# Kernel optimization log

Measured on AMD Instinct MI355X. Metric: run time of the kernel, lower is better.

The kernel has to match this reference:

```python
import jax, jax.numpy as jnp
import numpy as np

B, D, L = 16, 64, 1280
H = 8            # nhead
WIN = 5          # window_size (divides L exactly)
DFF = 128        # dim_feedforward
EPS = 1e-5


def _layernorm(x, g, b):
    mu = jnp.mean(x, axis=-1, keepdims=True)
    var = jnp.mean(jnp.square(x - mu), axis=-1, keepdims=True)
    return (x - mu) * jax.lax.rsqrt(var + EPS) * g + b


def _mha(x, w_in, b_in, w_out, b_out):
    # x: (Bx, Lx, D). torch nn.MultiheadAttention, batch_first, eval mode.
    Bx, Lx, Dm = x.shape
    hd = Dm // H
    qkv = x @ w_in.T + b_in                      # (Bx, Lx, 3D)
    q, k, v = jnp.split(qkv, 3, axis=-1)
    q = q.reshape(Bx, Lx, H, hd)
    k = k.reshape(Bx, Lx, H, hd)
    v = v.reshape(Bx, Lx, H, hd)
    scale = 1.0 / jnp.sqrt(jnp.asarray(hd, x.dtype))
    scores = jnp.einsum('bqhd,bkhd->bhqk', q, k) * scale
    att = jax.nn.softmax(scores, axis=-1)
    out = jnp.einsum('bhqk,bkhd->bqhd', att, v).reshape(Bx, Lx, Dm)
    return out @ w_out.T + b_out


def setup_inputs() -> dict:
    key = jax.random.key(0)
    ks = jax.random.split(key, 16)
    s = 0.05
    return {
        'x': jax.random.normal(ks[0], (B, D, L), dtype=jnp.float32),
        # local attention params
        'lw_in': jax.random.normal(ks[1], (3 * D, D), dtype=jnp.float32) * s,
        'lb_in': jnp.zeros((3 * D,), jnp.float32),
        'lw_out': jax.random.normal(ks[2], (D, D), dtype=jnp.float32) * s,
        'lb_out': jnp.zeros((D,), jnp.float32),
        # global attention params
        'gw_in': jax.random.normal(ks[3], (3 * D, D), dtype=jnp.float32) * s,
        'gb_in': jnp.zeros((3 * D,), jnp.float32),
        'gw_out': jax.random.normal(ks[4], (D, D), dtype=jnp.float32) * s,
        'gb_out': jnp.zeros((D,), jnp.float32),
        # gating weight (init 0.5 like the module)
        'local_weight': jnp.full((D,), 0.5, jnp.float32),
        # layer norms
        'g1': jnp.ones((D,), jnp.float32), 'b1': jnp.zeros((D,), jnp.float32),
        'g2': jnp.ones((D,), jnp.float32), 'b2': jnp.zeros((D,), jnp.float32),
        'g3': jnp.ones((D,), jnp.float32), 'b3': jnp.zeros((D,), jnp.float32),
        # FFN
        'w1': jax.random.normal(ks[5], (DFF, D), dtype=jnp.float32) * s,
        'bf1': jnp.zeros((DFF,), jnp.float32),
        'w2': jax.random.normal(ks[6], (D, DFF), dtype=jnp.float32) * s,
        'bf2': jnp.zeros((D,), jnp.float32),
    }


def reference(x, lw_in, lb_in, lw_out, lb_out, gw_in, gb_in, gw_out, gb_out,
              local_weight, g1, b1, g2, b2, g3, b3, w1, bf1, w2, bf2):
    xt = jnp.transpose(x, (0, 2, 1))              # (B, L, D)
    residual = xt
    nW = L // WIN
    xw = xt.reshape(B * nW, WIN, D)
    local_out = _mha(xw, lw_in, lb_in, lw_out, lb_out).reshape(B, L, D)
    local_out = _layernorm(local_out + residual, g1, b1)
    # global attention
    global_out = _mha(xt, gw_in, gb_in, gw_out, gb_out)
    global_out = _layernorm(global_out + residual, g2, b2)
    # gated channel fusion
    alpha = jax.nn.sigmoid(local_weight)[None, None, :]
    fused = alpha * local_out + (1.0 - alpha) * global_out
    # FFN (dropout is identity in eval mode)
    ffn_out = jax.nn.relu(fused @ w1.T + bf1) @ w2.T + bf2
    out = _layernorm(ffn_out + fused, g3, b3)
    return jnp.transpose(out, (0, 2, 1))          # (B, D, L)
```

## Files before the change

### kernel.cpp

```cpp
#include <hip/hip_runtime.h>
#include <math.h>

typedef short bf16x8 __attribute__((ext_vector_type(8)));
typedef float f32x4 __attribute__((ext_vector_type(4)));
typedef unsigned short u16;
typedef unsigned int u32;

#define RFL(x) __builtin_amdgcn_readfirstlane(x)

static __device__ __forceinline__ float bf2f(u16 s) {
  union { u32 u; float f; } c; c.u = ((u32)s) << 16; return c.f;
}
static __device__ __forceinline__ u16 f2bf(float f) {
  union { float f; u32 u; } c; c.f = f;
  u32 u = c.u + 0x7fffu + ((c.u >> 16) & 1u);
  return (u16)(u >> 16);
}
static __device__ __forceinline__ u32 pk2(float lo, float hi) {
  u32 r;
  asm("v_cvt_pk_bf16_f32 %0, %1, %2" : "=v"(r) : "v"(lo), "v"(hi));
  return r;
}
static __device__ __forceinline__ f32x4 MF(bf16x8 a, bf16x8 b, f32x4 c) {
  return __builtin_amdgcn_mfma_f32_16x16x32_bf16(a, b, c, 0, 0, 0);
}


__global__ __launch_bounds__(256) void qkvx(
    const float* __restrict__ x, const float* __restrict__ lw_in,
    const float* __restrict__ gw_in, const float* __restrict__ lb_in,
    const float* __restrict__ gb_in, u16* __restrict__ QKV) {
  __shared__ __align__(16) float xs[32][68];
  __shared__ __align__(16) u16 XTs[32 * 64];
  const int t = threadIdx.x;
  const int b = blockIdx.x / 40, l0 = (blockIdx.x % 40) * 32;
  for (int i = t; i < 2048; i += 256) {
    const int d = i >> 5, tok = i & 31;
    xs[tok][d] = x[(b * 64 + d) * 1280 + l0 + tok];
  }
  __syncthreads();
  {
    const int tok = t >> 3, c8 = (t & 7) * 8;
    union { bf16x8 v; u32 u[4]; } o;
    const float* src = &xs[tok][c8];
    o.u[0] = pk2(src[0], src[1]); o.u[1] = pk2(src[2], src[3]);
    o.u[2] = pk2(src[4], src[5]); o.u[3] = pk2(src[6], src[7]);
    const int byteoff = (tok * 128 + c8 * 2) ^ ((tok & 7) << 4);
    *(bf16x8*)((char*)XTs + byteoff) = o.v;
  }
  __syncthreads();
  const int lane = t & 63, w = RFL(t >> 6);
  const int lr = lane & 15, lg = lane >> 4;
  const int n0 = w * 96;
  bf16x8 a[2][2];
#pragma unroll
  for (int mt = 0; mt < 2; ++mt)
#pragma unroll
    for (int ks = 0; ks < 2; ++ks) {
      const int row = mt * 16 + lr;
      const int abyte = (row * 128 + ks * 64 + lg * 16) ^ ((row & 7) << 4);
      a[mt][ks] = *(const bf16x8*)((char*)XTs + abyte);
    }
  const float* W32 = (n0 < 192) ? lw_in : gw_in;
  const int nb = (n0 < 192) ? n0 : n0 - 192;
  bf16x8 bb[6][2];
#pragma unroll
  for (int nt = 0; nt < 6; ++nt)
#pragma unroll
    for (int ks = 0; ks < 2; ++ks) {
      const float* src = W32 + (nb + nt * 16 + lr) * 64 + ks * 32 + lg * 8;
      const float4 f0 = *(const float4*)src;
      const float4 f1 = *(const float4*)(src + 4);
      union { bf16x8 v; u32 u[4]; } o;
      o.u[0] = pk2(f0.x, f0.y); o.u[1] = pk2(f0.z, f0.w);
      o.u[2] = pk2(f1.x, f1.y); o.u[3] = pk2(f1.z, f1.w);
      bb[nt][ks] = o.v;
    }
  f32x4 acc[2][6];
#pragma unroll
  for (int mt = 0; mt < 2; ++mt)
#pragma unroll
    for (int nt = 0; nt < 6; ++nt) {
      f32x4 z = {0.f, 0.f, 0.f, 0.f};
      acc[mt][nt] = z;
#pragma unroll
      for (int ks = 0; ks < 2; ++ks)
        acc[mt][nt] = MF(a[mt][ks], bb[nt][ks], acc[mt][nt]);
    }
#pragma unroll
  for (int nt = 0; nt < 6; ++nt) {
    const int col = n0 + nt * 16 + lr;
    const float bias = (col < 192) ? lb_in[col] : gb_in[col - 192];
    const float scale = (col < 64) ? 0.35355339059327373f
                      : ((col >= 192 && col < 256) ? 0.51010407600615432f : 1.f);
#pragma unroll
    for (int mt = 0; mt < 2; ++mt)
#pragma unroll
      for (int r = 0; r < 4; ++r) {
        const int row = b * 1280 + l0 + mt * 16 + 4 * lg + r;
        QKV[row * 384 + col] = f2bf((acc[mt][nt][r] + bias) * scale);
      }
  }
}

__global__ __launch_bounds__(512) void attn(
    const u16* __restrict__ QKV, u16* __restrict__ AOl, u16* __restrict__ AOg,
    const float* __restrict__ lw_out, const float* __restrict__ gw_out,
    const float* __restrict__ w1, const float* __restrict__ w2,
    u16* __restrict__ Wlout, u16* __restrict__ Wgout,
    u16* __restrict__ W1b, u16* __restrict__ W2b) {
  __shared__ __align__(16) u16 Klds[1280 * 8];
  __shared__ __align__(16) u16 VT[9 * 1320];
  const int t = threadIdx.x;
  if (blockIdx.x < 10) {
    const int b = blockIdx.y >> 3, h = blockIdx.y & 7;
    for (int l = t; l < 1280; l += 512) {
      const int src = (b * 1280 + l) * 384 + h * 8;
      bf16x8 kv = *(const bf16x8*)(QKV + src + 256);
      bf16x8 vv = *(const bf16x8*)(QKV + src + 320);
      const int k5 = l & 31;
      const int pos = (l & ~31) + (((k5 >> 2) & 1) << 4) + (k5 & 3) + ((k5 >> 3) << 2);
      *(bf16x8*)(Klds + pos * 8) = kv;
#pragma unroll
      for (int d = 0; d < 8; ++d) VT[d * 1320 + l] = (u16)vv[d];
    }
    for (int l = t; l < 1320; l += 512) VT[8 * 1320 + l] = 0x3F80;
    __syncthreads();
    const int lane = t & 63, w = RFL(t >> 6);
    const int c = lane & 15, lg = lane >> 4;
    const int q0 = blockIdx.x * 128 + w * 16;
    const int qrow = b * 1280 + q0 + c;
    const bf16x8 qv = *(const bf16x8*)(QKV + qrow * 384 + 192 + h * 8);
    const bf16x8 qz = {0, 0, 0, 0, 0, 0, 0, 0};
    const bf16x8 qf = (lg == 0) ? qv : qz;
    const u16* kp = Klds + c * 8;
    const int vrow = (c < 8) ? c : 8;
    const u16* vp = VT + vrow * 1320 + lg * 8;
    f32x4 oacc = {0.f, 0.f, 0.f, 0.f};
#pragma unroll 4
    for (int jt = 0; jt < 40; ++jt) {
      bf16x8 kf0 = *(const bf16x8*)kp;
      bf16x8 kf1 = *(const bf16x8*)(kp + 128);
      f32x4 z = {0.f, 0.f, 0.f, 0.f};
      f32x4 s0 = MF(kf0, qf, z);
      f32x4 s1 = MF(kf1, qf, z);
      const float p0 = __builtin_amdgcn_exp2f(s0[0]);
      const float p1 = __builtin_amdgcn_exp2f(s0[1]);
      const float p2 = __builtin_amdgcn_exp2f(s0[2]);
      const float p3 = __builtin_amdgcn_exp2f(s0[3]);
      const float p4 = __builtin_amdgcn_exp2f(s1[0]);
      const float p5 = __builtin_amdgcn_exp2f(s1[1]);
      const float p6 = __builtin_amdgcn_exp2f(s1[2]);
      const float p7 = __builtin_amdgcn_exp2f(s1[3]);
      union { u32 u[4]; bf16x8 v; } pb;
      pb.u[0] = pk2(p0, p1);
      pb.u[1] = pk2(p2, p3);
      pb.u[2] = pk2(p4, p5);
      pb.u[3] = pk2(p6, p7);
      bf16x8 vf = *(const bf16x8*)vp;
      oacc = MF(vf, pb.v, oacc);
      kp += 256; vp += 32;
    }
    const float ssum = __shfl(oacc[0], 32 + c);
    const float inv = 1.f / ssum;
    if (lg < 2) {
      const int base = qrow * 64 + h * 8 + lg * 4;
      *(u32*)(AOg + base) = pk2(oacc[0] * inv, oacc[1] * inv);
      *(u32*)(AOg + base + 2) = pk2(oacc[2] * inv, oacc[3] * inv);
    }
    return;
  }
  const int lid = (blockIdx.x - 10) * 128 + blockIdx.y;
  if (lid < 320) {
    const int g = lid * 512 + t;
    const int qi = g % 5, h = (g / 5) & 7, wi = (g / 40) & 255, b = g / 10240;
    const int row = b * 1280 + wi * 5 + qi;
    float q[8];
    {
      bf16x8 qv = *(const bf16x8*)(QKV + row * 384 + h * 8);
#pragma unroll
      for (int d = 0; d < 8; ++d) q[d] = bf2f((u16)qv[d]);
    }
    float p[5], sum = 0.f;
#pragma unroll
    for (int j = 0; j < 5; ++j) {
      const int krow = b * 1280 + wi * 5 + j;
      bf16x8 kv = *(const bf16x8*)(QKV + krow * 384 + 64 + h * 8);
      float s = 0.f;
#pragma unroll
      for (int d = 0; d < 8; ++d) s = fmaf(q[d], bf2f((u16)kv[d]), s);
      p[j] = __expf(s); sum += p[j];
    }
    const float inv = 1.f / sum;
    float o[8] = {0, 0, 0, 0, 0, 0, 0, 0};
#pragma unroll
    for (int j = 0; j < 5; ++j) {
      const int vrow = b * 1280 + wi * 5 + j;
      bf16x8 vv = *(const bf16x8*)(QKV + vrow * 384 + 128 + h * 8);
#pragma unroll
      for (int d = 0; d < 8; ++d) o[d] = fmaf(p[j], bf2f((u16)vv[d]), o[d]);
    }
    union { bf16x8 v; u32 u[4]; } ov;
    ov.u[0] = pk2(o[0] * inv, o[1] * inv); ov.u[1] = pk2(o[2] * inv, o[3] * inv);
    ov.u[2] = pk2(o[4] * inv, o[5] * inv); ov.u[3] = pk2(o[6] * inv, o[7] * inv);
    *(bf16x8*)(AOl + row * 64 + h * 8) = ov.v;
  } else {
    const int f = (lid - 320) * 512 + t;
    if (f < 4096)       Wlout[f] = f2bf(lw_out[f]);
    else if (f < 8192)  Wgout[f - 4096] = f2bf(gw_out[f - 4096]);
    else if (f < 16384) W1b[f - 8192] = f2bf(w1[f - 8192]);
    else if (f < 24576) W2b[f - 16384] = f2bf(w2[f - 16384]);
  }
}

__global__ __launch_bounds__(64) void tail_kernel(
    const u16* __restrict__ AOl, const u16* __restrict__ AOg,
    const u16* __restrict__ Wlout, const u16* __restrict__ Wgout,
    const u16* __restrict__ W1b, const u16* __restrict__ W2b,
    const float* __restrict__ lb_out, const float* __restrict__ gb_out,
    const float* __restrict__ lwt,
    const float* __restrict__ g1, const float* __restrict__ b1,
    const float* __restrict__ g2, const float* __restrict__ b2,
    const float* __restrict__ g3, const float* __restrict__ b3,
    const float* __restrict__ bf1, const float* __restrict__ bf2,
    const float* __restrict__ x, float* __restrict__ out) {
  __shared__ __align__(16) float xso[64][20];
  __shared__ __align__(16) u16 Ft[16 * 64];
  __shared__ __align__(16) u16 Ht[16 * 128];
  const int t = threadIdx.x;
  const int b = blockIdx.y, l0 = blockIdx.x * 16;
  for (int i = t; i < 1024; i += 64) {
    const int d = i >> 4, tok = i & 15;
    xso[d][tok] = x[(b * 64 + d) * 1280 + l0 + tok];
  }
  __syncthreads();
  const int lr = t & 15, lg = (t & 63) >> 4;
  const int grow = b * 1280 + l0;

  f32x4 accl[4], accg[4];
#pragma unroll
  for (int nt = 0; nt < 4; ++nt) { f32x4 z = {0,0,0,0}; accl[nt] = z; accg[nt] = z; }
#pragma unroll
  for (int ks = 0; ks < 2; ++ks) {
    bf16x8 al = *(const bf16x8*)(AOl + (grow + lr) * 64 + ks * 32 + lg * 8);
    bf16x8 ag = *(const bf16x8*)(AOg + (grow + lr) * 64 + ks * 32 + lg * 8);
#pragma unroll
    for (int nt = 0; nt < 4; ++nt) {
      bf16x8 bl = *(const bf16x8*)(Wlout + (nt * 16 + lr) * 64 + ks * 32 + lg * 8);
      bf16x8 bg = *(const bf16x8*)(Wgout + (nt * 16 + lr) * 64 + ks * 32 + lg * 8);
      accl[nt] = MF(al, bl, accl[nt]);
      accg[nt] = MF(ag, bg, accg[nt]);
    }
  }
#pragma unroll
  for (int nt = 0; nt < 4; ++nt) {
    const int col = nt * 16 + lr;
    const float bl = lb_out[col], bg = gb_out[col];
    f32x4 xr = *(const f32x4*)&xso[col][lg * 4];
#pragma unroll
    for (int r = 0; r < 4; ++r) {
      accl[nt][r] += bl + xr[r];
      accg[nt][r] += bg + xr[r];
    }
  }
  auto LN = [&](f32x4* a, const float* gam, const float* bet) {
    float gv[4], bv[4];
#pragma unroll
    for (int nt = 0; nt < 4; ++nt) { gv[nt] = gam[nt * 16 + lr]; bv[nt] = bet[nt * 16 + lr]; }
#pragma unroll
    for (int r = 0; r < 4; ++r) {
      float s = a[0][r] + a[1][r] + a[2][r] + a[3][r];
      s += __shfl_xor(s, 1); s += __shfl_xor(s, 2);
      s += __shfl_xor(s, 4); s += __shfl_xor(s, 8);
      const float mu = s * 0.015625f;
      float q = 0.f;
#pragma unroll
      for (int nt = 0; nt < 4; ++nt) { const float cv = a[nt][r] - mu; q = fmaf(cv, cv, q); }
      q += __shfl_xor(q, 1); q += __shfl_xor(q, 2);
      q += __shfl_xor(q, 4); q += __shfl_xor(q, 8);
      const float rsq = rsqrtf(q * 0.015625f + 1e-5f);
#pragma unroll
      for (int nt = 0; nt < 4; ++nt)
        a[nt][r] = (a[nt][r] - mu) * rsq * gv[nt] + bv[nt];
    }
  };
  LN(accl, g1, b1);
  LN(accg, g2, b2);
  f32x4 fus[4];
#pragma unroll
  for (int nt = 0; nt < 4; ++nt) {
    const int col = nt * 16 + lr;
    const float al_ = 1.f / (1.f + __expf(-lwt[col]));
#pragma unroll
    for (int r = 0; r < 4; ++r)
      fus[nt][r] = al_ * accl[nt][r] + (1.f - al_) * accg[nt][r];
  }
#pragma unroll
  for (int nt = 0; nt < 4; ++nt)
#pragma unroll
    for (int r = 0; r < 4; ++r) {
      const int ltok = lg * 4 + r;
      const int byteoff = (ltok * 128 + (nt * 16 + lr) * 2) ^ ((ltok & 7) << 4);
      *(u16*)((char*)Ft + byteoff) = f2bf(fus[nt][r]);
    }
  asm volatile("" ::: "memory");
  __syncthreads();
  f32x4 hcc[8];
#pragma unroll
  for (int nt = 0; nt < 8; ++nt) { f32x4 z = {0,0,0,0}; hcc[nt] = z; }
#pragma unroll
  for (int ks = 0; ks < 2; ++ks) {
    const int abyte = (lr * 128 + ks * 64 + lg * 16) ^ ((lr & 7) << 4);
    bf16x8 af = *(const bf16x8*)((char*)Ft + abyte);
#pragma unroll
    for (int nt = 0; nt < 8; ++nt) {
      bf16x8 bw = *(const bf16x8*)(W1b + (nt * 16 + lr) * 64 + ks * 32 + lg * 8);
      hcc[nt] = MF(af, bw, hcc[nt]);
    }
  }
#pragma unroll
  for (int nt = 0; nt < 8; ++nt) {
    const int f = nt * 16 + lr;
    const float bbv = bf1[f];
#pragma unroll
    for (int r = 0; r < 4; ++r) {
      const float v = fmaxf(hcc[nt][r] + bbv, 0.f);
      const int ltok = lg * 4 + r;
      const int byteoff = (ltok * 256 + f * 2) ^ ((ltok & 7) << 4);
      *(u16*)((char*)Ht + byteoff) = f2bf(v);
    }
  }
  asm volatile("" ::: "memory");
  f32x4 occ[4];
#pragma unroll
  for (int nt = 0; nt < 4; ++nt) { f32x4 z = {0,0,0,0}; occ[nt] = z; }
#pragma unroll
  for (int ks = 0; ks < 4; ++ks) {
    const int abyte = (lr * 256 + ks * 64 + lg * 16) ^ ((lr & 7) << 4);
    bf16x8 af = *(const bf16x8*)((char*)Ht + abyte);
#pragma unroll
    for (int nt = 0; nt < 4; ++nt) {
      bf16x8 bw = *(const bf16x8*)(W2b + (nt * 16 + lr) * 128 + ks * 32 + lg * 8);
      occ[nt] = MF(af, bw, occ[nt]);
    }
  }
#pragma unroll
  for (int nt = 0; nt < 4; ++nt) {
    const float bb2 = bf2[nt * 16 + lr];
#pragma unroll
    for (int r = 0; r < 4; ++r) occ[nt][r] += bb2 + fus[nt][r];
  }
  LN(occ, g3, b3);
#pragma unroll
  for (int nt = 0; nt < 4; ++nt)
#pragma unroll
    for (int r = 0; r < 4; ++r)
      xso[nt * 16 + lr][lg * 4 + r] = occ[nt][r];
  __syncthreads();
  for (int i = t; i < 1024; i += 64) {
    const int d = i >> 4, tok = i & 15;
    out[(b * 64 + d) * 1280 + l0 + tok] = xso[d][tok];
  }
}

extern "C" void kernel_launch(void* const* d_in, const int* in_sizes, int n_in,
                              void* d_out, int out_size, void* d_ws,
                              size_t ws_size, hipStream_t stream) {
  const float* x      = (const float*)d_in[0];
  const float* lw_in  = (const float*)d_in[1];
  const float* lb_in  = (const float*)d_in[2];
  const float* lw_out = (const float*)d_in[3];
  const float* lb_out = (const float*)d_in[4];
  const float* gw_in  = (const float*)d_in[5];
  const float* gb_in  = (const float*)d_in[6];
  const float* gw_out = (const float*)d_in[7];
  const float* gb_out = (const float*)d_in[8];
  const float* lwt    = (const float*)d_in[9];
  const float* g1 = (const float*)d_in[10]; const float* b1 = (const float*)d_in[11];
  const float* g2 = (const float*)d_in[12]; const float* b2 = (const float*)d_in[13];
  const float* g3 = (const float*)d_in[14]; const float* b3 = (const float*)d_in[15];
  const float* w1 = (const float*)d_in[16]; const float* bf1 = (const float*)d_in[17];
  const float* w2 = (const float*)d_in[18]; const float* bf2 = (const float*)d_in[19];
  float* out = (float*)d_out;

  u16* QKV   = (u16*)d_ws;
  u16* AOl   = QKV + 7864320;
  u16* AOg   = AOl + 1310720;
  u16* Wlout = AOg + 1310720;
  u16* Wgout = Wlout + 4096;
  u16* W1b   = Wgout + 4096;
  u16* W2b   = W1b + 8192;

  qkvx<<<dim3(640), dim3(256), 0, stream>>>(x, lw_in, gw_in, lb_in, gb_in, QKV);
  attn<<<dim3(13, 128), dim3(512), 0, stream>>>(QKV, AOl, AOg, lw_out, gw_out,
                                                w1, w2, Wlout, Wgout, W1b, W2b);
  tail_kernel<<<dim3(80, 16), dim3(64), 0, stream>>>(
      AOl, AOg, Wlout, Wgout, W1b, W2b, lb_out, gb_out, lwt,
      g1, b1, g2, b2, g3, b3, bf1, bf2, x, out);
}
```

Measured before the change: 73.86 us.

## Use 32x32x16 MFMA for global attention with 32 queries per wave

```diff
diff --git a/kernel.cpp b/kernel.cpp
--- a/kernel.cpp
+++ b/kernel.cpp
@@ -3,6 +3,7 @@
 
 typedef short bf16x8 __attribute__((ext_vector_type(8)));
 typedef float f32x4 __attribute__((ext_vector_type(4)));
+typedef float f32x16 __attribute__((ext_vector_type(16)));
 typedef unsigned short u16;
 typedef unsigned int u32;
 
@@ -23,6 +24,9 @@
 }
 static __device__ __forceinline__ f32x4 MF(bf16x8 a, bf16x8 b, f32x4 c) {
   return __builtin_amdgcn_mfma_f32_16x16x32_bf16(a, b, c, 0, 0, 0);
+}
+static __device__ __forceinline__ f32x16 MF32(bf16x8 a, bf16x8 b, f32x16 c) {
+  return __builtin_amdgcn_mfma_f32_32x32x16_bf16(a, b, c, 0, 0, 0);
 }
 
 
@@ -112,65 +116,63 @@
   __shared__ __align__(16) u16 Klds[1280 * 8];
   __shared__ __align__(16) u16 VT[9 * 1320];
   const int t = threadIdx.x;
-  if (blockIdx.x < 10) {
+  if (blockIdx.x < 5) {
     const int b = blockIdx.y >> 3, h = blockIdx.y & 7;
     for (int l = t; l < 1280; l += 512) {
       const int src = (b * 1280 + l) * 384 + h * 8;
       bf16x8 kv = *(const bf16x8*)(QKV + src + 256);
       bf16x8 vv = *(const bf16x8*)(QKV + src + 320);
       const int k5 = l & 31;
-      const int pos = (l & ~31) + (((k5 >> 2) & 1) << 4) + (k5 & 3) + ((k5 >> 3) << 2);
+      const int pos = (l & ~31) +
+                      ((k5 & 0x13) | ((k5 & 4) << 1) | ((k5 & 8) >> 1));
       *(bf16x8*)(Klds + pos * 8) = kv;
 #pragma unroll
       for (int d = 0; d < 8; ++d) VT[d * 1320 + l] = (u16)vv[d];
     }
-    for (int l = t; l < 1320; l += 512) VT[8 * 1320 + l] = 0x3F80;
+    for (int l = t; l < 1280; l += 512) VT[8 * 1320 + l] = 0x3F80;
     __syncthreads();
     const int lane = t & 63, w = RFL(t >> 6);
-    const int c = lane & 15, lg = lane >> 4;
-    const int q0 = blockIdx.x * 128 + w * 16;
+    const int c = lane & 31, hi = lane >> 5;
+    const int q0 = blockIdx.x * 256 + w * 32;
     const int qrow = b * 1280 + q0 + c;
     const bf16x8 qv = *(const bf16x8*)(QKV + qrow * 384 + 192 + h * 8);
     const bf16x8 qz = {0, 0, 0, 0, 0, 0, 0, 0};
-    const bf16x8 qf = (lg == 0) ? qv : qz;
+    const bf16x8 qf = (hi == 0) ? qv : qz;
     const u16* kp = Klds + c * 8;
     const int vrow = (c < 8) ? c : 8;
-    const u16* vp = VT + vrow * 1320 + lg * 8;
-    f32x4 oacc = {0.f, 0.f, 0.f, 0.f};
-#pragma unroll 4
+    const u16* vp = VT + vrow * 1320 + hi * 8;
+    f32x16 oacc;
+#pragma unroll
+    for (int i = 0; i < 16; ++i) oacc[i] = 0.f;
+    f32x16 z16;
+#pragma unroll
+    for (int i = 0; i < 16; ++i) z16[i] = 0.f;
+#pragma unroll 2
     for (int jt = 0; jt < 40; ++jt) {
-      bf16x8 kf0 = *(const bf16x8*)kp;
-      bf16x8 kf1 = *(const bf16x8*)(kp + 128);
-      f32x4 z = {0.f, 0.f, 0.f, 0.f};
-      f32x4 s0 = MF(kf0, qf, z);
-      f32x4 s1 = MF(kf1, qf, z);
-      const float p0 = __builtin_amdgcn_exp2f(s0[0]);
-      const float p1 = __builtin_amdgcn_exp2f(s0[1]);
-      const float p2 = __builtin_amdgcn_exp2f(s0[2]);
-      const float p3 = __builtin_amdgcn_exp2f(s0[3]);
-      const float p4 = __builtin_amdgcn_exp2f(s1[0]);
-      const float p5 = __builtin_amdgcn_exp2f(s1[1]);
-      const float p6 = __builtin_amdgcn_exp2f(s1[2]);
-      const float p7 = __builtin_amdgcn_exp2f(s1[3]);
-      union { u32 u[4]; bf16x8 v; } pb;
-      pb.u[0] = pk2(p0, p1);
-      pb.u[1] = pk2(p2, p3);
-      pb.u[2] = pk2(p4, p5);
-      pb.u[3] = pk2(p6, p7);
-      bf16x8 vf = *(const bf16x8*)vp;
-      oacc = MF(vf, pb.v, oacc);
+      bf16x8 kf = *(const bf16x8*)kp;
+      f32x16 s = MF32(kf, qf, z16);
+      float p[16];
+#pragma unroll
+      for (int i = 0; i < 16; ++i) p[i] = __builtin_amdgcn_exp2f(s[i]);
+      union { u32 u[4]; bf16x8 v; } pb1, pb2;
+      pb1.u[0] = pk2(p[0], p[1]);  pb1.u[1] = pk2(p[2], p[3]);
+      pb1.u[2] = pk2(p[4], p[5]);  pb1.u[3] = pk2(p[6], p[7]);
+      pb2.u[0] = pk2(p[8], p[9]);  pb2.u[1] = pk2(p[10], p[11]);
+      pb2.u[2] = pk2(p[12], p[13]); pb2.u[3] = pk2(p[14], p[15]);
+      bf16x8 vf1 = *(const bf16x8*)vp;
+      oacc = MF32(vf1, pb1.v, oacc);
+      bf16x8 vf2 = *(const bf16x8*)(vp + 16);
+      oacc = MF32(vf2, pb2.v, oacc);
       kp += 256; vp += 32;
     }
-    const float ssum = __shfl(oacc[0], 32 + c);
+    const float ssum = __shfl(oacc[4], c);
     const float inv = 1.f / ssum;
-    if (lg < 2) {
-      const int base = qrow * 64 + h * 8 + lg * 4;
-      *(u32*)(AOg + base) = pk2(oacc[0] * inv, oacc[1] * inv);
-      *(u32*)(AOg + base + 2) = pk2(oacc[2] * inv, oacc[3] * inv);
-    }
+    const int base = qrow * 64 + h * 8 + hi * 4;
+    *(u32*)(AOg + base) = pk2(oacc[0] * inv, oacc[1] * inv);
+    *(u32*)(AOg + base + 2) = pk2(oacc[2] * inv, oacc[3] * inv);
     return;
   }
-  const int lid = (blockIdx.x - 10) * 128 + blockIdx.y;
+  const int lid = (blockIdx.x - 5) * 128 + blockIdx.y;
   if (lid < 320) {
     const int g = lid * 512 + t;
     const int qi = g % 5, h = (g / 5) & 7, wi = (g / 40) & 255, b = g / 10240;
@@ -392,8 +394,8 @@
   u16* W2b   = W1b + 8192;
 
   qkvx<<<dim3(640), dim3(256), 0, stream>>>(x, lw_in, gw_in, lb_in, gb_in, QKV);
-  attn<<<dim3(13, 128), dim3(512), 0, stream>>>(QKV, AOl, AOg, lw_out, gw_out,
-                                                w1, w2, Wlout, Wgout, W1b, W2b);
+  attn<<<dim3(8, 128), dim3(512), 0, stream>>>(QKV, AOl, AOg, lw_out, gw_out,
+                                               w1, w2, Wlout, Wgout, W1b, W2b);
   tail_kernel<<<dim3(80, 16), dim3(64), 0, stream>>>(
       AOl, AOg, Wlout, Wgout, W1b, W2b, lb_out, gb_out, lwt,
       g1, b1, g2, b2, g3, b3, bf1, bf2, x, out);
```

After: 77.03 us. 4.3% more time.
